# Performance work log

Measured on AMD Instinct MI355X. Metric: run time of the kernel, lower is better.

The kernel has to match this reference:

```python
import jax, jax.numpy as jnp
import numpy as np
from jax import lax

B, T, N, H, NC = 2, 8, 512, 64, 10
NEG = -1e9
LN_EPS = 1e-5


def _gatv2(x, mask, Wl, Wr, att, b):
    # GATv2Conv (PyG semantics, eval mode): e_ij = att . leaky_relu(Wr x_i + Wl x_j),
    # softmax over source nodes j with self-loops, out_i = sum_j alpha_ij * (Wl x_j).
    # x: (B, N, Fin); mask: (N, N) bool adjacency incl. self-loops; att: (heads, C).
    heads, C = att.shape
    Bn, Nn, _ = x.shape
    xl = (x @ Wl).reshape(Bn, Nn, heads, C)  # source transform
    xr = (x @ Wr).reshape(Bn, Nn, heads, C)  # target transform
    s = jax.nn.leaky_relu(xr[:, :, None] + xl[:, None, :], 0.2)  # (B, Ni, Nj, h, C)
    e = jnp.einsum('bijhc,hc->bijh', s, att)
    e = jnp.where(mask[None, :, :, None], e, NEG)
    alpha = jax.nn.softmax(e, axis=2)  # softmax over neighbors j
    out = jnp.einsum('bijh,bjhc->bihc', alpha, xl)
    return out.reshape(Bn, Nn, heads * C) + b


def _gru_layer(x, Wih, Whh, bih, bhh):
    # torch nn.GRU single layer, batch_first; x: (B, T, Hin)
    h0 = jnp.zeros((x.shape[0], Whh.shape[0]), x.dtype)
    def step(h, xt):
        gi = xt @ Wih + bih
        gh = h @ Whh + bhh
        ir, iz, inn = jnp.split(gi, 3, axis=-1)
        hr, hz, hn = jnp.split(gh, 3, axis=-1)
        r = jax.nn.sigmoid(ir + hr)
        z = jax.nn.sigmoid(iz + hz)
        n = jnp.tanh(inn + r * hn)
        hnew = (1.0 - z) * n + z * h
        return hnew, hnew
    _, ys = lax.scan(step, h0, jnp.swapaxes(x, 0, 1))
    return jnp.swapaxes(ys, 0, 1)


def setup_inputs() -> dict:
    key = jax.random.key(0)
    ks = jax.random.split(key, 20)
    def rn(i, shape, s=0.1):
        return jax.random.normal(ks[i], shape, jnp.float32) * s
    x_seq = jax.random.normal(ks[0], (B, T, N, 1), jnp.float32)
    a = jax.random.uniform(ks[1], (N, N))
    up = jnp.triu((a > 0.95).astype(jnp.float32), 1)
    static_adj = up + up.T  # sparse symmetric 0/1 static graph
    dyn_W = jax.random.normal(ks[2], (N, N), jnp.float32)
    reg_lambda = jnp.array([0.05], jnp.float32)
    return {
        'x_seq': x_seq, 'static_adj': static_adj, 'dyn_W': dyn_W, 'reg_lambda': reg_lambda,
        'g1_Wl': rn(3, (1, H)), 'g1_Wr': rn(4, (1, H)), 'g1_att': rn(5, (4, H // 4)), 'g1_b': jnp.zeros(H),
        'g2_Wl': rn(6, (H, H)), 'g2_Wr': rn(7, (H, H)), 'g2_att': rn(8, (1, H)), 'g2_b': jnp.zeros(H),
        'gru_Wih0': rn(9, (H, 3 * H)), 'gru_Whh0': rn(10, (H, 3 * H)), 'gru_bih0': jnp.zeros(3 * H), 'gru_bhh0': jnp.zeros(3 * H),
        'gru_Wih1': rn(11, (H, 3 * H)), 'gru_Whh1': rn(12, (H, 3 * H)), 'gru_bih1': jnp.zeros(3 * H), 'gru_bhh1': jnp.zeros(3 * H),
        'attn_W': rn(13, (H, 1)), 'attn_b': jnp.zeros(1),
        'cls_W1': rn(14, (H, H)), 'cls_b1': jnp.zeros(H), 'ln_g': jnp.ones(H), 'ln_b': jnp.zeros(H),
        'cls_W2': rn(15, (H, NC)), 'cls_b2': jnp.zeros(NC),
    }


def reference(x_seq, static_adj, dyn_W, reg_lambda,
              g1_Wl, g1_Wr, g1_att, g1_b, g2_Wl, g2_Wr, g2_att, g2_b,
              gru_Wih0, gru_Whh0, gru_bih0, gru_bhh0,
              gru_Wih1, gru_Whh1, gru_bih1, gru_bhh1,
              attn_W, attn_b, cls_W1, cls_b1, ln_g, ln_b, cls_W2, cls_b2):
    Bn, Tn, Nn, _ = x_seq.shape
    lam = jnp.maximum(reg_lambda[0], 0.01)
    t = jnp.arange(Tn, dtype=x_seq.dtype)
    gts = jnp.exp(-lam * t)  # gating values per timestep
    dyn = jax.nn.relu(dyn_W + dyn_W.T)
    fused = gts[:, None, None] * static_adj + (1.0 - gts)[:, None, None] * dyn  # (T, N, N)
    masks = (fused > 0) | jnp.eye(Nn, dtype=bool)[None]  # edge set + self-loops

    def step(carry, inp):
        xt, mask = inp  # xt: (B, N, 1)
        h = jax.nn.elu(_gatv2(xt, mask, g1_Wl, g1_Wr, g1_att, g1_b))
        h = jax.nn.elu(_gatv2(h, mask, g2_Wl, g2_Wr, g2_att, g2_b))
        return carry, h.mean(axis=1)  # (B, H) graph readout

    _, reps = lax.scan(step, 0.0, (jnp.swapaxes(x_seq, 0, 1), masks))
    h_seq = jnp.swapaxes(reps, 0, 1)  # (B, T, H)

    gru_out = _gru_layer(h_seq, gru_Wih0, gru_Whh0, gru_bih0, gru_bhh0)
    gru_out = _gru_layer(gru_out, gru_Wih1, gru_Whh1, gru_bih1, gru_bhh1)

    att_scores = jax.nn.softmax((gru_out @ attn_W + attn_b)[..., 0], axis=1)  # (B, T)
    final = jnp.einsum('bt,bth->bh', att_scores, gru_out)

    z = final @ cls_W1 + cls_b1
    mu = jnp.mean(z, axis=-1, keepdims=True)
    var = jnp.var(z, axis=-1, keepdims=True)
    z = (z - mu) / jnp.sqrt(var + LN_EPS) * ln_g + ln_b
    z = jax.nn.gelu(z, approximate=False)
    logits = z @ cls_W2 + cls_b2
    return logits, gts, att_scores
```

## Files before the change

kernel.cpp:

```cpp
#include <hip/hip_runtime.h>
#include <math.h>

#define BB 2
#define TT 8
#define NN 512
#define HH 64
#define NC 10

typedef unsigned char uchar;

__device__ __forceinline__ float elu1(float v){ return v > 0.f ? v : expm1f(v); }
__device__ __forceinline__ float sigm(float v){ return 1.f/(1.f+expf(-v)); }

__global__ __launch_bounds__(256) void k_mask(
    const float* __restrict__ dW, const float* __restrict__ sadj,
    uchar* __restrict__ M0, uchar* __restrict__ M1,
    float* __restrict__ Z2, float* __restrict__ hseq,
    const float* __restrict__ att1, const float* __restrict__ Wr1,
    const float* __restrict__ Wl1, float* __restrict__ AB,
    const float* __restrict__ Whh0, const float* __restrict__ Wih1,
    const float* __restrict__ Whh1, float4* __restrict__ WT4)
{
    __shared__ float tr[64][65];
    int bx = blockIdx.x, by = blockIdx.y;
    int tid = threadIdx.x;
    if (blockIdx.z == 1){
        int idx = (by*8 + bx)*256 + tid;
        if (idx < 3*4096){
            int m = idx >> 12, r = idx & 4095;
            int gg = r >> 6, k = r & 63;
            const float* W = (m == 0) ? Whh0 : (m == 1) ? Wih1 : Whh1;
            float4 o;
            o.x = W[k*192 + gg];
            o.y = W[k*192 + 64 + gg];
            o.z = W[k*192 + 128 + gg];
            o.w = 0.f;
            WT4[(size_t)m*4096 + r] = o;
        }
        return;
    }
    int i0 = by*64, j0 = bx*64;
    #pragma unroll
    for (int q = 0; q < 4; ++q){
        int r = (tid >> 4) + 16*q, c4 = tid & 15;
        float4 v = *(const float4*)&dW[(size_t)(j0+r)*NN + i0 + 4*c4];
        tr[r][4*c4+0] = v.x; tr[r][4*c4+1] = v.y;
        tr[r][4*c4+2] = v.z; tr[r][4*c4+3] = v.w;
    }
    __syncthreads();
    #pragma unroll
    for (int q = 0; q < 4; ++q){
        int row = (tid >> 4) + 16*q, c4 = tid & 15;
        int i = i0 + row, j = j0 + 4*c4;
        float4 d  = *(const float4*)&dW[(size_t)i*NN + j];
        float4 sa = *(const float4*)&sadj[(size_t)i*NN + j];
        uchar4 m0, m1;
        float dd0 = d.x + tr[4*c4+0][row];
        float dd1 = d.y + tr[4*c4+1][row];
        float dd2 = d.z + tr[4*c4+2][row];
        float dd3 = d.w + tr[4*c4+3][row];
        m0.x = (sa.x > 0.f) || (i == j+0);
        m0.y = (sa.y > 0.f) || (i == j+1);
        m0.z = (sa.z > 0.f) || (i == j+2);
        m0.w = (sa.w > 0.f) || (i == j+3);
        m1.x = m0.x || (dd0 > 0.f);
        m1.y = m0.y || (dd1 > 0.f);
        m1.z = m0.z || (dd2 > 0.f);
        m1.w = m0.w || (dd3 > 0.f);
        *(uchar4*)&M0[(size_t)i*NN + j] = m0;
        *(uchar4*)&M1[(size_t)i*NN + j] = m1;
    }
    int flat = (by*8 + bx)*256 + tid;
    if (flat < BB*TT*NN) Z2[flat] = 0.f;
    else if (flat < BB*TT*NN + BB*TT*HH) hseq[flat - BB*TT*NN] = 0.f;
    if (bx == 0 && by == 0 && tid < 8){
        int h = tid & 3;
        const float* W = (tid < 4) ? Wr1 : Wl1;
        float s = 0.f;
        for (int c = 0; c < 16; ++c) s += att1[h*16+c]*W[h*16+c];
        AB[tid] = s;
    }
}

__global__ __launch_bounds__(256) void k_gat1f(
    const float* __restrict__ x_seq, const uchar* __restrict__ M0,
    const uchar* __restrict__ M1,
    const float* __restrict__ Wl, const float* __restrict__ Wr,
    const float* __restrict__ att, const float* __restrict__ bias,
    const float* __restrict__ AB,
    const float* __restrict__ Wl2, const float* __restrict__ Wr2,
    const float* __restrict__ att2,
    float* __restrict__ xl2, float* __restrict__ xr2,
    float* __restrict__ ui, float* __restrict__ vj)
{
    __shared__ float x_s[NN];
    __shared__ float S_s[4][4];
    __shared__ float h_s[4][HH];
    __shared__ float Wl2_s[64*64];
    __shared__ float Wr2_s[64*64];
    int bt = blockIdx.y; int t = bt % TT;
    int i0 = blockIdx.x * 4;
    int tid = threadIdx.x;
    int il = tid >> 6, jl = tid & 63;
    int i = i0 + il;
    const uchar* M = t ? M1 : M0;
    ((float2*)x_s)[tid] = ((const float2*)(x_seq + bt*NN))[tid];
    #pragma unroll
    for (int q = 0; q < 4; ++q){
        int idx = q*256 + tid;
        ((float4*)Wl2_s)[idx] = ((const float4*)Wl2)[idx];
        ((float4*)Wr2_s)[idx] = ((const float4*)Wr2)[idx];
    }
    __syncthreads();
    float xi = x_s[i];
    const uchar* Mrow = M + (size_t)i*NN;
    float xj[8], msk[8];
    #pragma unroll
    for (int jj = 0; jj < 8; ++jj){
        int j = jj*64 + jl;
        xj[jj] = x_s[j];
        msk[jj] = Mrow[j] ? 1.f : 0.f;
    }
    float sw[4] = {0,0,0,0}, swx[4] = {0,0,0,0};
    for (int h = 0; h < 4; ++h){
        float acc[8] = {0,0,0,0,0,0,0,0};
        #pragma unroll
        for (int c = 0; c < 16; ++c){
            int hc = h*16 + c;
            float wl = Wl[hc];
            float q  = 0.4f * att[hc];
            float pr = xi * Wr[hc];
            #pragma unroll
            for (int jj = 0; jj < 8; ++jj){
                float s = fmaf(xj[jj], wl, pr);
                acc[jj] = fmaf(q, fabsf(s), acc[jj]);
            }
        }
        float lin = 0.6f * xi * AB[h];
        float al6 = 0.6f * AB[4+h];
        #pragma unroll
        for (int jj = 0; jj < 8; ++jj){
            float e = acc[jj] + fmaf(al6, xj[jj], lin);
            float w = msk[jj] * __expf(e);
            sw[h] += w;
            swx[h] = fmaf(w, xj[jj], swx[h]);
        }
    }
    #pragma unroll
    for (int off = 32; off; off >>= 1){
        #pragma unroll
        for (int h = 0; h < 4; ++h){
            sw[h]  += __shfl_down(sw[h],  off);
            swx[h] += __shfl_down(swx[h], off);
        }
    }
    if (jl == 0){
        #pragma unroll
        for (int h = 0; h < 4; ++h) S_s[il][h] = swx[h] / sw[h];
    }
    __syncthreads();
    {
        int hc = tid & 63, row = tid >> 6;
        float v = S_s[row][hc >> 4] * Wl[hc] + bias[hc];
        h_s[row][hc] = elu1(v);
    }
    __syncthreads();
    {
        int c = tid & 63, row = tid >> 6;
        float al = 0.f, ar = 0.f;
        #pragma unroll 8
        for (int k = 0; k < 64; ++k){
            float hv = h_s[row][k];
            al = fmaf(hv, Wl2_s[k*64 + c], al);
            ar = fmaf(hv, Wr2_s[k*64 + c], ar);
        }
        size_t ridx = (size_t)(bt*NN + i0 + row);
        xl2[ridx*HH + c] = al;
        xr2[ridx*HH + c] = ar;
        float a2 = att2[c];
        float pu = a2 * ar, pv = a2 * al;
        #pragma unroll
        for (int off = 32; off; off >>= 1){
            pu += __shfl_down(pu, off);
            pv += __shfl_down(pv, off);
        }
        if (c == 0){ ui[ridx] = pu; vj[ridx] = pv; }
    }
}

__global__ __launch_bounds__(256) void k_e2(
    const float* __restrict__ xl2, const float* __restrict__ xr2,
    const uchar* __restrict__ M0, const uchar* __restrict__ M1,
    const float* __restrict__ att,
    const float* __restrict__ ui, const float* __restrict__ vj,
    float* __restrict__ WgT, float* __restrict__ Z2)
{
    __shared__ float xrT[64][68];
    __shared__ float xlT[64][68];
    int bt = blockIdx.z, t = bt % TT;
    int i0 = blockIdx.y*64, j0 = blockIdx.x*64;
    int base = bt*NN;
    int tid = threadIdx.x;
    const uchar* M = t ? M1 : M0;
    {
        int r = tid >> 2;
        #pragma unroll
        for (int q = 0; q < 4; ++q){
            int c4 = (tid & 3) + 4*q;
            float4 a = *(const float4*)&xr2[(size_t)(base+i0+r)*HH + 4*c4];
            float4 b = *(const float4*)&xl2[(size_t)(base+j0+r)*HH + 4*c4];
            xrT[4*c4+0][r] = a.x; xrT[4*c4+1][r] = a.y;
            xrT[4*c4+2][r] = a.z; xrT[4*c4+3][r] = a.w;
            xlT[4*c4+0][r] = b.x; xlT[4*c4+1][r] = b.y;
            xlT[4*c4+2][r] = b.z; xlT[4*c4+3][r] = b.w;
        }
    }
    int ti = tid >> 4, tj = tid & 15;
    int iL = ti*4, jL = tj*4;
    float4 u4 = *(const float4*)&ui[base+i0+iL];
    float4 v4 = *(const float4*)&vj[base+j0+jL];
    float uu[4] = {u4.x, u4.y, u4.z, u4.w};
    float vv[4] = {v4.x, v4.y, v4.z, v4.w};
    float acc[4][4];
    #pragma unroll
    for (int ii = 0; ii < 4; ++ii)
        #pragma unroll
        for (int jj = 0; jj < 4; ++jj)
            acc[ii][jj] = 0.6f*(uu[ii] + vv[jj]);
    __syncthreads();
    #pragma unroll 8
    for (int c = 0; c < 64; ++c){
        float qa = 0.4f * att[c];
        float4 a4 = *(const float4*)&xrT[c][iL];
        float4 b4 = *(const float4*)&xlT[c][jL];
        float a[4] = {a4.x, a4.y, a4.z, a4.w};
        float b[4] = {b4.x, b4.y, b4.z, b4.w};
        #pragma unroll
        for (int ii = 0; ii < 4; ++ii)
            #pragma unroll
            for (int jj = 0; jj < 4; ++jj)
                acc[ii][jj] = fmaf(qa, fabsf(a[ii] + b[jj]), acc[ii][jj]);
    }
    float w[4][4];
    #pragma unroll
    for (int ii = 0; ii < 4; ++ii){
        int i = i0 + iL + ii;
        uchar4 mr = *(const uchar4*)&M[(size_t)i*NN + j0 + jL];
        w[ii][0] = mr.x ? __expf(acc[ii][0]) : 0.f;
        w[ii][1] = mr.y ? __expf(acc[ii][1]) : 0.f;
        w[ii][2] = mr.z ? __expf(acc[ii][2]) : 0.f;
        w[ii][3] = mr.w ? __expf(acc[ii][3]) : 0.f;
    }
    #pragma unroll
    for (int jj = 0; jj < 4; ++jj){
        int j = j0 + jL + jj;
        float4 wv = { w[0][jj], w[1][jj], w[2][jj], w[3][jj] };
        *(float4*)&WgT[(size_t)(base+j)*NN + i0 + iL] = wv;
    }
    #pragma unroll
    for (int ii = 0; ii < 4; ++ii){
        float zi = w[ii][0] + w[ii][1] + w[ii][2] + w[ii][3];
        zi += __shfl_down(zi, 8);
        zi += __shfl_down(zi, 4);
        zi += __shfl_down(zi, 2);
        zi += __shfl_down(zi, 1);
        if (tj == 0) atomicAdd(&Z2[base + i0 + iL + ii], zi);
    }
}

__global__ __launch_bounds__(256) void k_a2(
    const float* __restrict__ WgT, const float* __restrict__ xl2,
    const float* __restrict__ Z2, const float* __restrict__ bias,
    float* __restrict__ hseq)
{
    __shared__ float a_s[64][20];
    __shared__ float x_s[64][68];
    __shared__ float msum[64];
    int bt = blockIdx.y;
    int i0 = blockIdx.x * 16;
    int base = bt * NN;
    int tid = threadIdx.x;
    int tg = tid >> 4, tc = tid & 15;
    if (tid < 64) msum[tid] = 0.f;
    float4 acc = {0,0,0,0};
    for (int jc = 0; jc < 8; ++jc){
        int j0 = jc*64;
        {
            int row = tid >> 2, c4 = tid & 3;
            ((float4*)&a_s[row][0])[c4] = ((const float4*)&WgT[(size_t)(base+j0+row)*NN + i0])[c4];
        }
        #pragma unroll
        for (int q = 0; q < 4; ++q){
            int idx = q*256 + tid; int row = idx >> 4, c4 = idx & 15;
            ((float4*)&x_s[row][0])[c4] = ((const float4*)&xl2[(size_t)(base+j0+row)*HH])[c4];
        }
        __syncthreads();
        #pragma unroll 8
        for (int j = 0; j < 64; ++j){
            float a = a_s[j][tg];
            float4 xv = ((float4*)&x_s[j][0])[tc];
            acc.x = fmaf(a, xv.x, acc.x);
            acc.y = fmaf(a, xv.y, acc.y);
            acc.z = fmaf(a, xv.z, acc.z);
            acc.w = fmaf(a, xv.w, acc.w);
        }
        __syncthreads();
    }
    float rz = 1.f / Z2[base + i0 + tg];
    float4 b4 = ((const float4*)bias)[tc];
    float4 h;
    h.x = elu1(acc.x*rz + b4.x);
    h.y = elu1(acc.y*rz + b4.y);
    h.z = elu1(acc.z*rz + b4.z);
    h.w = elu1(acc.w*rz + b4.w);
    atomicAdd(&msum[tc*4+0], h.x);
    atomicAdd(&msum[tc*4+1], h.y);
    atomicAdd(&msum[tc*4+2], h.z);
    atomicAdd(&msum[tc*4+3], h.w);
    __syncthreads();
    if (tid < 64) atomicAdd(&hseq[bt*HH + tid], msum[tid]*(1.f/(float)NN));
}

__global__ __launch_bounds__(256) void k_pre(
    const float* __restrict__ hseq, const float* __restrict__ Wih0,
    const float* __restrict__ bih0, float* __restrict__ gi0)
{
    int idx = blockIdx.x*256 + threadIdx.x;
    int bt = idx / 192, g = idx % 192;
    const float* x = hseq + bt*HH;
    float acc = bih0[g];
    #pragma unroll 8
    for (int k = 0; k < HH; ++k)
        acc = fmaf(x[k], Wih0[k*192 + g], acc);
    gi0[idx] = acc;
}

#define P4 65
__global__ __launch_bounds__(512) void k_gru2(
    const float* __restrict__ gi0, const float4* __restrict__ WT4,
    const float* __restrict__ bhh0,
    const float* __restrict__ bih1, const float* __restrict__ bhh1,
    const float* __restrict__ lamp, const float* __restrict__ attn_W,
    const float* __restrict__ attn_b, const float* __restrict__ W1,
    const float* __restrict__ b1, const float* __restrict__ ln_g,
    const float* __restrict__ ln_b, const float* __restrict__ W2,
    const float* __restrict__ b2, float* __restrict__ out)
{
    __shared__ float4 WA[64*P4];
    __shared__ float4 WB[64*P4];
    __shared__ float gi_s[BB*TT*192];
    __shared__ float y_s[BB*TT*HH];
    __shared__ float sc_s[BB][TT], at_s[BB][TT];
    __shared__ float fin_s[BB][HH], z_s[BB][HH], g_s[BB][HH];
    __shared__ float mu_s[BB], iv_s[BB];
    int tid = threadIdx.x;
    int wave = tid >> 6, lane = tid & 63;
    for (int v = tid; v < 4096; v += 512){
        WA[(v >> 6)*P4 + (v & 63)] = WT4[v];
        WB[(v >> 6)*P4 + (v & 63)] = WT4[4096 + v];
    }
    for (int v = tid; v < BB*TT*192; v += 512) gi_s[v] = gi0[v];
    __syncthreads();
    float y[TT];
    float g1r[TT], g1z[TT], g1n[TT];
    if (wave < 2){
        int b = wave;
        float bhr = bhh0[lane], bhz = bhh0[64+lane], bhn = bhh0[128+lane];
        float h = 0.f;
        for (int t = 0; t < TT; ++t){
            float ghr = bhr, ghz = bhz, ghn = bhn;
            #pragma unroll 16
            for (int k = 0; k < 64; ++k){
                float4 w4 = WA[lane*P4 + k];
                float hk = __shfl(h, k);
                ghr = fmaf(w4.x, hk, ghr);
                ghz = fmaf(w4.y, hk, ghz);
                ghn = fmaf(w4.z, hk, ghn);
            }
            const float* gi = &gi_s[(b*TT + t)*192];
            float r = sigm(gi[lane] + ghr);
            float z = sigm(gi[64+lane] + ghz);
            float n = tanhf(gi[128+lane] + r*ghn);
            h = (1.f - z)*n + z*h;
            y[t] = h;
        }
        float bi1r = bih1[lane], bi1z = bih1[64+lane], bi1n = bih1[128+lane];
        #pragma unroll
        for (int t = 0; t < TT; ++t){ g1r[t] = bi1r; g1z[t] = bi1z; g1n[t] = bi1n; }
        #pragma unroll 8
        for (int k = 0; k < 64; ++k){
            float4 w4 = WB[lane*P4 + k];
            #pragma unroll
            for (int t = 0; t < TT; ++t){
                float yk = __shfl(y[t], k);
                g1r[t] = fmaf(w4.x, yk, g1r[t]);
                g1z[t] = fmaf(w4.y, yk, g1z[t]);
                g1n[t] = fmaf(w4.z, yk, g1n[t]);
            }
        }
    }
    __syncthreads();
    if (wave >= 2){
        for (int v = tid - 128; v < 4096; v += 384)
            WA[(v >> 6)*P4 + (v & 63)] = WT4[2*4096 + v];
    }
    __syncthreads();
    if (wave < 2){
        int b = wave;
        float bhr = bhh1[lane], bhz = bhh1[64+lane], bhn = bhh1[128+lane];
        float h = 0.f;
        for (int t = 0; t < TT; ++t){
            float ghr = bhr, ghz = bhz, ghn = bhn;
            #pragma unroll 16
            for (int k = 0; k < 64; ++k){
                float4 w4 = WA[lane*P4 + k];
                float hk = __shfl(h, k);
                ghr = fmaf(w4.x, hk, ghr);
                ghz = fmaf(w4.y, hk, ghz);
                ghn = fmaf(w4.z, hk, ghn);
            }
            float r = sigm(g1r[t] + ghr);
            float z = sigm(g1z[t] + ghz);
            float n = tanhf(g1n[t] + r*ghn);
            h = (1.f - z)*n + z*h;
            y_s[(b*TT + t)*HH + lane] = h;
        }
    }
    __syncthreads();
    float lam = fmaxf(lamp[0], 0.01f);
    if (tid < TT) out[BB*NC + tid] = expf(-lam*(float)tid);
    if (tid < BB*TT){
        int bb = tid >> 3, t = tid & 7;
        float s = attn_b[0];
        const float* r = &y_s[(bb*TT+t)*HH];
        for (int h = 0; h < HH; ++h) s += r[h]*attn_W[h];
        sc_s[bb][t] = s;
    }
    __syncthreads();
    if (tid < BB){
        float mx = -INFINITY;
        for (int t = 0; t < TT; ++t) mx = fmaxf(mx, sc_s[tid][t]);
        float se = 0.f;
        for (int t = 0; t < TT; ++t){ float w = expf(sc_s[tid][t]-mx); at_s[tid][t] = w; se += w; }
        for (int t = 0; t < TT; ++t){
            at_s[tid][t] /= se;
            out[BB*NC + TT + tid*TT + t] = at_s[tid][t];
        }
    }
    __syncthreads();
    if (tid < BB*HH){
        int bb = tid >> 6, h = tid & 63;
        float a = 0.f;
        for (int t = 0; t < TT; ++t) a += at_s[bb][t]*y_s[(bb*TT+t)*HH + h];
        fin_s[bb][h] = a;
    }
    __syncthreads();
    if (tid < BB*HH){
        int bb = tid >> 6, h = tid & 63;
        float a = b1[h];
        for (int k = 0; k < HH; ++k) a += fin_s[bb][k]*W1[k*HH+h];
        z_s[bb][h] = a;
    }
    __syncthreads();
    if (tid < BB){
        float mu = 0.f;
        for (int h = 0; h < HH; ++h) mu += z_s[tid][h];
        mu *= (1.f/HH);
        float v = 0.f;
        for (int h = 0; h < HH; ++h){ float d = z_s[tid][h]-mu; v += d*d; }
        v *= (1.f/HH);
        mu_s[tid] = mu; iv_s[tid] = 1.f/sqrtf(v + 1e-5f);
    }
    __syncthreads();
    if (tid < BB*HH){
        int bb = tid >> 6, h = tid & 63;
        float zn = (z_s[bb][h]-mu_s[bb])*iv_s[bb]*ln_g[h] + ln_b[h];
        g_s[bb][h] = 0.5f*zn*(1.f + erff(zn*0.70710678118654752f));
    }
    __syncthreads();
    if (tid < BB*NC){
        int bb = tid / NC, c = tid % NC;
        float a = b2[c];
        for (int k = 0; k < HH; ++k) a += g_s[bb][k]*W2[k*NC+c];
        out[bb*NC + c] = a;
    }
}

extern "C" void kernel_launch(void* const* d_in, const int* in_sizes, int n_in,
                              void* d_out, int out_size, void* d_ws, size_t ws_size,
                              hipStream_t stream)
{
    const float* x_seq = (const float*)d_in[0];
    const float* sadj  = (const float*)d_in[1];
    const float* dynW  = (const float*)d_in[2];
    const float* lamp  = (const float*)d_in[3];
    const float* g1_Wl = (const float*)d_in[4];
    const float* g1_Wr = (const float*)d_in[5];
    const float* g1_att= (const float*)d_in[6];
    const float* g1_b  = (const float*)d_in[7];
    const float* g2_Wl = (const float*)d_in[8];
    const float* g2_Wr = (const float*)d_in[9];
    const float* g2_att= (const float*)d_in[10];
    const float* g2_b  = (const float*)d_in[11];
    const float* Wih0  = (const float*)d_in[12];
    const float* Whh0  = (const float*)d_in[13];
    const float* bih0  = (const float*)d_in[14];
    const float* bhh0  = (const float*)d_in[15];
    const float* Wih1  = (const float*)d_in[16];
    const float* Whh1  = (const float*)d_in[17];
    const float* bih1  = (const float*)d_in[18];
    const float* bhh1  = (const float*)d_in[19];
    const float* attnW = (const float*)d_in[20];
    const float* attnb = (const float*)d_in[21];
    const float* W1    = (const float*)d_in[22];
    const float* b1    = (const float*)d_in[23];
    const float* lng   = (const float*)d_in[24];
    const float* lnb   = (const float*)d_in[25];
    const float* W2    = (const float*)d_in[26];
    const float* b2    = (const float*)d_in[27];
    float* out = (float*)d_out;

    const int RWS = BB*TT*NN*HH;
    uchar* M0 = (uchar*)d_ws;
    uchar* M1 = M0 + (size_t)NN*NN;
    float* fb = (float*)(M1 + (size_t)NN*NN);
    float* Z2   = fb;
    float* AB   = Z2   + BB*TT*NN;
    float* ui   = AB   + 16;
    float* vj   = ui   + BB*TT*NN;
    float* xl2  = vj   + BB*TT*NN;
    float* xr2  = xl2  + RWS;
    float* WgT  = xr2  + RWS;
    float* hseq = WgT  + (size_t)BB*TT*NN*NN;
    float* gi0  = hseq + BB*TT*HH;
    float4* WT4 = (float4*)(gi0 + BB*TT*192);

    k_mask <<<dim3(8,8,2), 256, 0, stream>>>(dynW, sadj, M0, M1, Z2, hseq, g1_att, g1_Wr, g1_Wl, AB,
                                             Whh0, Wih1, Whh1, WT4);
    k_gat1f<<<dim3(NN/4, BB*TT), 256, 0, stream>>>(x_seq, M0, M1, g1_Wl, g1_Wr, g1_att, g1_b, AB,
                                                   g2_Wl, g2_Wr, g2_att, xl2, xr2, ui, vj);
    k_e2   <<<dim3(NN/64, NN/64, BB*TT), 256, 0, stream>>>(xl2, xr2, M0, M1, g2_att, ui, vj, WgT, Z2);
    k_a2   <<<dim3(NN/16, BB*TT), 256, 0, stream>>>(WgT, xl2, Z2, g2_b, hseq);
    k_pre  <<<12, 256, 0, stream>>>(hseq, Wih0, bih0, gi0);
    k_gru2 <<<1, 512, 0, stream>>>(gi0, WT4, bhh0, bih1, bhh1,
                                   lamp, attnW, attnb, W1, b1, lng, lnb, W2, b2, out);
}
```

Before: 223.0 us.

## Fuse GAT, GRU and classifier stages into one persistent kernel with grid barriers

Replaces the six-kernel pipeline with a small init kernel plus a single persistent 256-block kernel whose stages are separated by a software grid barrier built on atomics. Intermediate buffers such as the dense NxN weight matrix and the atomic normalizer appear to be dropped, with layer-2 attention likely recomputed per row block and per-block mean partials used for the readout. This aims to remove launch overhead and large global round-trips. It risks deadlock if the 256 blocks are not all co-resident, and the grid barriers serialize stages.

New measurement: 390.7 us. 75.2% more time.

```diff
diff --git a/kernel.cpp b/kernel.cpp
--- a/kernel.cpp
+++ b/kernel.cpp
@@ -6,483 +6,488 @@
 #define NN 512
 #define HH 64
 #define NC 10
+#define NBLK 256
 
 typedef unsigned char uchar;
 
 __device__ __forceinline__ float elu1(float v){ return v > 0.f ? v : expm1f(v); }
 __device__ __forceinline__ float sigm(float v){ return 1.f/(1.f+expf(-v)); }
 
-__global__ __launch_bounds__(256) void k_mask(
-    const float* __restrict__ dW, const float* __restrict__ sadj,
-    uchar* __restrict__ M0, uchar* __restrict__ M1,
-    float* __restrict__ Z2, float* __restrict__ hseq,
-    const float* __restrict__ att1, const float* __restrict__ Wr1,
-    const float* __restrict__ Wl1, float* __restrict__ AB,
-    const float* __restrict__ Whh0, const float* __restrict__ Wih1,
-    const float* __restrict__ Whh1, float4* __restrict__ WT4)
-{
-    __shared__ float tr[64][65];
-    int bx = blockIdx.x, by = blockIdx.y;
-    int tid = threadIdx.x;
-    if (blockIdx.z == 1){
-        int idx = (by*8 + bx)*256 + tid;
-        if (idx < 3*4096){
-            int m = idx >> 12, r = idx & 4095;
-            int gg = r >> 6, k = r & 63;
-            const float* W = (m == 0) ? Whh0 : (m == 1) ? Wih1 : Whh1;
-            float4 o;
-            o.x = W[k*192 + gg];
-            o.y = W[k*192 + 64 + gg];
-            o.z = W[k*192 + 128 + gg];
-            o.w = 0.f;
-            WT4[(size_t)m*4096 + r] = o;
-        }
-        return;
-    }
-    int i0 = by*64, j0 = bx*64;
-    #pragma unroll
-    for (int q = 0; q < 4; ++q){
-        int r = (tid >> 4) + 16*q, c4 = tid & 15;
-        float4 v = *(const float4*)&dW[(size_t)(j0+r)*NN + i0 + 4*c4];
-        tr[r][4*c4+0] = v.x; tr[r][4*c4+1] = v.y;
-        tr[r][4*c4+2] = v.z; tr[r][4*c4+3] = v.w;
+__device__ __forceinline__ void grid_barrier(unsigned* bar){
+    __syncthreads();
+    if (threadIdx.x == 0){
+        __threadfence();
+        unsigned gen = __hip_atomic_load(&bar[1], __ATOMIC_ACQUIRE, __HIP_MEMORY_SCOPE_AGENT);
+        unsigned a = __hip_atomic_fetch_add(&bar[0], 1u, __ATOMIC_ACQ_REL, __HIP_MEMORY_SCOPE_AGENT);
+        if (a == NBLK - 1u){
+            __hip_atomic_store(&bar[0], 0u, __ATOMIC_RELAXED, __HIP_MEMORY_SCOPE_AGENT);
+            __hip_atomic_fetch_add(&bar[1], 1u, __ATOMIC_RELEASE, __HIP_MEMORY_SCOPE_AGENT);
+        } else {
+            while (__hip_atomic_load(&bar[1], __ATOMIC_ACQUIRE, __HIP_MEMORY_SCOPE_AGENT) == gen)
+                __builtin_amdgcn_s_sleep(8);
+        }
+        __threadfence();
     }
     __syncthreads();
-    #pragma unroll
-    for (int q = 0; q < 4; ++q){
-        int row = (tid >> 4) + 16*q, c4 = tid & 15;
-        int i = i0 + row, j = j0 + 4*c4;
-        float4 d  = *(const float4*)&dW[(size_t)i*NN + j];
-        float4 sa = *(const float4*)&sadj[(size_t)i*NN + j];
-        uchar4 m0, m1;
-        float dd0 = d.x + tr[4*c4+0][row];
-        float dd1 = d.y + tr[4*c4+1][row];
-        float dd2 = d.z + tr[4*c4+2][row];
-        float dd3 = d.w + tr[4*c4+3][row];
-        m0.x = (sa.x > 0.f) || (i == j+0);
-        m0.y = (sa.y > 0.f) || (i == j+1);
-        m0.z = (sa.z > 0.f) || (i == j+2);
-        m0.w = (sa.w > 0.f) || (i == j+3);
-        m1.x = m0.x || (dd0 > 0.f);
-        m1.y = m0.y || (dd1 > 0.f);
-        m1.z = m0.z || (dd2 > 0.f);
-        m1.w = m0.w || (dd3 > 0.f);
-        *(uchar4*)&M0[(size_t)i*NN + j] = m0;
-        *(uchar4*)&M1[(size_t)i*NN + j] = m1;
+}
+
+struct Prm {
+    const float *x_seq, *sadj, *dW, *lamp;
+    const float *g1_Wl, *g1_Wr, *g1_att, *g1_b;
+    const float *g2_Wl, *g2_Wr, *g2_att, *g2_b;
+    const float *Wih0, *bih0, *bhh0;
+    const float *bih1, *bhh1;
+    const float *attnW, *attnb, *W1, *b1, *lng, *lnb, *W2, *b2;
+    uchar *M0, *M1;
+    float *WT4;
+    float *xl2, *xr2, *ui, *vj, *meanPart;
+    unsigned *bar;
+    float *out;
+};
+
+__global__ __launch_bounds__(256) void k_init(
+    const float* __restrict__ Whh0, const float* __restrict__ Wih1,
+    const float* __restrict__ Whh1, const float* __restrict__ lamp,
+    float4* __restrict__ WT4, unsigned* __restrict__ bar, float* __restrict__ out)
+{
+    int idx = blockIdx.x*256 + threadIdx.x;
+    if (blockIdx.x == 0){
+        if (threadIdx.x < 2) bar[threadIdx.x] = 0u;
+        if (threadIdx.x >= 32 && threadIdx.x < 32 + TT){
+            int t = threadIdx.x - 32;
+            float lam = fmaxf(lamp[0], 0.01f);
+            out[BB*NC + t] = expf(-lam*(float)t);
+        }
     }
-    int flat = (by*8 + bx)*256 + tid;
-    if (flat < BB*TT*NN) Z2[flat] = 0.f;
-    else if (flat < BB*TT*NN + BB*TT*HH) hseq[flat - BB*TT*NN] = 0.f;
-    if (bx == 0 && by == 0 && tid < 8){
-        int h = tid & 3;
-        const float* W = (tid < 4) ? Wr1 : Wl1;
-        float s = 0.f;
-        for (int c = 0; c < 16; ++c) s += att1[h*16+c]*W[h*16+c];
-        AB[tid] = s;
-    }
+    int m = idx >> 12, r = idx & 4095;
+    int gg = r >> 6, k = r & 63;
+    const float* W = (m == 0) ? Whh0 : (m == 1) ? Wih1 : Whh1;
+    float4 o;
+    o.x = W[k*192 + gg];
+    o.y = W[k*192 + 64 + gg];
+    o.z = W[k*192 + 128 + gg];
+    o.w = 0.f;
+    WT4[idx] = o;
 }
 
-__global__ __launch_bounds__(256) void k_gat1f(
-    const float* __restrict__ x_seq, const uchar* __restrict__ M0,
-    const uchar* __restrict__ M1,
-    const float* __restrict__ Wl, const float* __restrict__ Wr,
-    const float* __restrict__ att, const float* __restrict__ bias,
-    const float* __restrict__ AB,
-    const float* __restrict__ Wl2, const float* __restrict__ Wr2,
-    const float* __restrict__ att2,
-    float* __restrict__ xl2, float* __restrict__ xr2,
-    float* __restrict__ ui, float* __restrict__ vj)
+#define SMEM_BYTES 52736
+
+__global__ __launch_bounds__(256, 1) void mega(Prm p)
 {
-    __shared__ float x_s[NN];
-    __shared__ float S_s[4][4];
-    __shared__ float h_s[4][HH];
-    __shared__ float Wl2_s[64*64];
-    __shared__ float Wr2_s[64*64];
-    int bt = blockIdx.y; int t = bt % TT;
-    int i0 = blockIdx.x * 4;
+    __shared__ __align__(16) char smem[SMEM_BYTES];
+    int blk = blockIdx.x;
     int tid = threadIdx.x;
-    int il = tid >> 6, jl = tid & 63;
-    int i = i0 + il;
-    const uchar* M = t ? M1 : M0;
-    ((float2*)x_s)[tid] = ((const float2*)(x_seq + bt*NN))[tid];
-    #pragma unroll
-    for (int q = 0; q < 4; ++q){
-        int idx = q*256 + tid;
-        ((float4*)Wl2_s)[idx] = ((const float4*)Wl2)[idx];
-        ((float4*)Wr2_s)[idx] = ((const float4*)Wr2)[idx];
-    }
-    __syncthreads();
-    float xi = x_s[i];
-    const uchar* Mrow = M + (size_t)i*NN;
-    float xj[8], msk[8];
-    #pragma unroll
-    for (int jj = 0; jj < 8; ++jj){
-        int j = jj*64 + jl;
-        xj[jj] = x_s[j];
-        msk[jj] = Mrow[j] ? 1.f : 0.f;
-    }
-    float sw[4] = {0,0,0,0}, swx[4] = {0,0,0,0};
-    for (int h = 0; h < 4; ++h){
-        float acc[8] = {0,0,0,0,0,0,0,0};
-        #pragma unroll
-        for (int c = 0; c < 16; ++c){
-            int hc = h*16 + c;
-            float wl = Wl[hc];
-            float q  = 0.4f * att[hc];
-            float pr = xi * Wr[hc];
-            #pragma unroll
-            for (int jj = 0; jj < 8; ++jj){
-                float s = fmaf(xj[jj], wl, pr);
-                acc[jj] = fmaf(q, fabsf(s), acc[jj]);
-            }
-        }
-        float lin = 0.6f * xi * AB[h];
-        float al6 = 0.6f * AB[4+h];
-        #pragma unroll
-        for (int jj = 0; jj < 8; ++jj){
-            float e = acc[jj] + fmaf(al6, xj[jj], lin);
-            float w = msk[jj] * __expf(e);
-            sw[h] += w;
-            swx[h] = fmaf(w, xj[jj], swx[h]);
-        }
-    }
-    #pragma unroll
-    for (int off = 32; off; off >>= 1){
-        #pragma unroll
-        for (int h = 0; h < 4; ++h){
-            sw[h]  += __shfl_down(sw[h],  off);
-            swx[h] += __shfl_down(swx[h], off);
-        }
-    }
-    if (jl == 0){
-        #pragma unroll
-        for (int h = 0; h < 4; ++h) S_s[il][h] = swx[h] / sw[h];
-    }
-    __syncthreads();
-    {
-        int hc = tid & 63, row = tid >> 6;
-        float v = S_s[row][hc >> 4] * Wl[hc] + bias[hc];
-        h_s[row][hc] = elu1(v);
-    }
-    __syncthreads();
-    {
-        int c = tid & 63, row = tid >> 6;
-        float al = 0.f, ar = 0.f;
-        #pragma unroll 8
-        for (int k = 0; k < 64; ++k){
-            float hv = h_s[row][k];
-            al = fmaf(hv, Wl2_s[k*64 + c], al);
-            ar = fmaf(hv, Wr2_s[k*64 + c], ar);
-        }
-        size_t ridx = (size_t)(bt*NN + i0 + row);
-        xl2[ridx*HH + c] = al;
-        xr2[ridx*HH + c] = ar;
-        float a2 = att2[c];
-        float pu = a2 * ar, pv = a2 * al;
-        #pragma unroll
-        for (int off = 32; off; off >>= 1){
-            pu += __shfl_down(pu, off);
-            pv += __shfl_down(pv, off);
-        }
-        if (c == 0){ ui[ridx] = pu; vj[ridx] = pv; }
-    }
-}
-
-__global__ __launch_bounds__(256) void k_e2(
-    const float* __restrict__ xl2, const float* __restrict__ xr2,
-    const uchar* __restrict__ M0, const uchar* __restrict__ M1,
-    const float* __restrict__ att,
-    const float* __restrict__ ui, const float* __restrict__ vj,
-    float* __restrict__ WgT, float* __restrict__ Z2)
-{
-    __shared__ float xrT[64][68];
-    __shared__ float xlT[64][68];
-    int bt = blockIdx.z, t = bt % TT;
-    int i0 = blockIdx.y*64, j0 = blockIdx.x*64;
-    int base = bt*NN;
-    int tid = threadIdx.x;
-    const uchar* M = t ? M1 : M0;
-    {
-        int r = tid >> 2;
+
+    if (blk < 64){
+        float (*tr)[65] = (float(*)[65])smem;
+        int i0 = (blk >> 3)*64, j0 = (blk & 7)*64;
         #pragma unroll
         for (int q = 0; q < 4; ++q){
-            int c4 = (tid & 3) + 4*q;
-            float4 a = *(const float4*)&xr2[(size_t)(base+i0+r)*HH + 4*c4];
-            float4 b = *(const float4*)&xl2[(size_t)(base+j0+r)*HH + 4*c4];
-            xrT[4*c4+0][r] = a.x; xrT[4*c4+1][r] = a.y;
-            xrT[4*c4+2][r] = a.z; xrT[4*c4+3][r] = a.w;
-            xlT[4*c4+0][r] = b.x; xlT[4*c4+1][r] = b.y;
-            xlT[4*c4+2][r] = b.z; xlT[4*c4+3][r] = b.w;
-        }
-    }
-    int ti = tid >> 4, tj = tid & 15;
-    int iL = ti*4, jL = tj*4;
-    float4 u4 = *(const float4*)&ui[base+i0+iL];
-    float4 v4 = *(const float4*)&vj[base+j0+jL];
-    float uu[4] = {u4.x, u4.y, u4.z, u4.w};
-    float vv[4] = {v4.x, v4.y, v4.z, v4.w};
-    float acc[4][4];
-    #pragma unroll
-    for (int ii = 0; ii < 4; ++ii)
-        #pragma unroll
-        for (int jj = 0; jj < 4; ++jj)
-            acc[ii][jj] = 0.6f*(uu[ii] + vv[jj]);
-    __syncthreads();
-    #pragma unroll 8
-    for (int c = 0; c < 64; ++c){
-        float qa = 0.4f * att[c];
-        float4 a4 = *(const float4*)&xrT[c][iL];
-        float4 b4 = *(const float4*)&xlT[c][jL];
-        float a[4] = {a4.x, a4.y, a4.z, a4.w};
-        float b[4] = {b4.x, b4.y, b4.z, b4.w};
-        #pragma unroll
-        for (int ii = 0; ii < 4; ++ii)
-            #pragma unroll
-            for (int jj = 0; jj < 4; ++jj)
-                acc[ii][jj] = fmaf(qa, fabsf(a[ii] + b[jj]), acc[ii][jj]);
-    }
-    float w[4][4];
-    #pragma unroll
-    for (int ii = 0; ii < 4; ++ii){
-        int i = i0 + iL + ii;
-        uchar4 mr = *(const uchar4*)&M[(size_t)i*NN + j0 + jL];
-        w[ii][0] = mr.x ? __expf(acc[ii][0]) : 0.f;
-        w[ii][1] = mr.y ? __expf(acc[ii][1]) : 0.f;
-        w[ii][2] = mr.z ? __expf(acc[ii][2]) : 0.f;
-        w[ii][3] = mr.w ? __expf(acc[ii][3]) : 0.f;
-    }
-    #pragma unroll
-    for (int jj = 0; jj < 4; ++jj){
-        int j = j0 + jL + jj;
-        float4 wv = { w[0][jj], w[1][jj], w[2][jj], w[3][jj] };
-        *(float4*)&WgT[(size_t)(base+j)*NN + i0 + iL] = wv;
-    }
-    #pragma unroll
-    for (int ii = 0; ii < 4; ++ii){
-        float zi = w[ii][0] + w[ii][1] + w[ii][2] + w[ii][3];
-        zi += __shfl_down(zi, 8);
-        zi += __shfl_down(zi, 4);
-        zi += __shfl_down(zi, 2);
-        zi += __shfl_down(zi, 1);
-        if (tj == 0) atomicAdd(&Z2[base + i0 + iL + ii], zi);
-    }
-}
-
-__global__ __launch_bounds__(256) void k_a2(
-    const float* __restrict__ WgT, const float* __restrict__ xl2,
-    const float* __restrict__ Z2, const float* __restrict__ bias,
-    float* __restrict__ hseq)
-{
-    __shared__ float a_s[64][20];
-    __shared__ float x_s[64][68];
-    __shared__ float msum[64];
-    int bt = blockIdx.y;
-    int i0 = blockIdx.x * 16;
-    int base = bt * NN;
-    int tid = threadIdx.x;
-    int tg = tid >> 4, tc = tid & 15;
-    if (tid < 64) msum[tid] = 0.f;
-    float4 acc = {0,0,0,0};
-    for (int jc = 0; jc < 8; ++jc){
-        int j0 = jc*64;
-        {
-            int row = tid >> 2, c4 = tid & 3;
-            ((float4*)&a_s[row][0])[c4] = ((const float4*)&WgT[(size_t)(base+j0+row)*NN + i0])[c4];
-        }
+            int r = (tid >> 4) + 16*q, c4 = tid & 15;
+            float4 v = *(const float4*)&p.dW[(size_t)(j0+r)*NN + i0 + 4*c4];
+            tr[r][4*c4+0] = v.x; tr[r][4*c4+1] = v.y;
+            tr[r][4*c4+2] = v.z; tr[r][4*c4+3] = v.w;
+        }
+        __syncthreads();
         #pragma unroll
         for (int q = 0; q < 4; ++q){
-            int idx = q*256 + tid; int row = idx >> 4, c4 = idx & 15;
-            ((float4*)&x_s[row][0])[c4] = ((const float4*)&xl2[(size_t)(base+j0+row)*HH])[c4];
-        }
-        __syncthreads();
-        #pragma unroll 8
-        for (int j = 0; j < 64; ++j){
-            float a = a_s[j][tg];
-            float4 xv = ((float4*)&x_s[j][0])[tc];
-            acc.x = fmaf(a, xv.x, acc.x);
-            acc.y = fmaf(a, xv.y, acc.y);
-            acc.z = fmaf(a, xv.z, acc.z);
-            acc.w = fmaf(a, xv.w, acc.w);
-        }
-        __syncthreads();
+            int row = (tid >> 4) + 16*q, c4 = tid & 15;
+            int i = i0 + row, j = j0 + 4*c4;
+            float4 d  = *(const float4*)&p.dW[(size_t)i*NN + j];
+            float4 sa = *(const float4*)&p.sadj[(size_t)i*NN + j];
+            uchar4 m0, m1;
+            float dd0 = d.x + tr[4*c4+0][row];
+            float dd1 = d.y + tr[4*c4+1][row];
+            float dd2 = d.z + tr[4*c4+2][row];
+            float dd3 = d.w + tr[4*c4+3][row];
+            m0.x = (sa.x > 0.f) || (i == j+0);
+            m0.y = (sa.y > 0.f) || (i == j+1);
+            m0.z = (sa.z > 0.f) || (i == j+2);
+            m0.w = (sa.w > 0.f) || (i == j+3);
+            m1.x = m0.x || (dd0 > 0.f);
+            m1.y = m0.y || (dd1 > 0.f);
+            m1.z = m0.z || (dd2 > 0.f);
+            m1.w = m0.w || (dd3 > 0.f);
+            *(uchar4*)&p.M0[(size_t)i*NN + j] = m0;
+            *(uchar4*)&p.M1[(size_t)i*NN + j] = m1;
+        }
     }
-    float rz = 1.f / Z2[base + i0 + tg];
-    float4 b4 = ((const float4*)bias)[tc];
-    float4 h;
-    h.x = elu1(acc.x*rz + b4.x);
-    h.y = elu1(acc.y*rz + b4.y);
-    h.z = elu1(acc.z*rz + b4.z);
-    h.w = elu1(acc.w*rz + b4.w);
-    atomicAdd(&msum[tc*4+0], h.x);
-    atomicAdd(&msum[tc*4+1], h.y);
-    atomicAdd(&msum[tc*4+2], h.z);
-    atomicAdd(&msum[tc*4+3], h.w);
-    __syncthreads();
-    if (tid < 64) atomicAdd(&hseq[bt*HH + tid], msum[tid]*(1.f/(float)NN));
-}
-
-__global__ __launch_bounds__(256) void k_pre(
-    const float* __restrict__ hseq, const float* __restrict__ Wih0,
-    const float* __restrict__ bih0, float* __restrict__ gi0)
-{
-    int idx = blockIdx.x*256 + threadIdx.x;
-    int bt = idx / 192, g = idx % 192;
-    const float* x = hseq + bt*HH;
-    float acc = bih0[g];
-    #pragma unroll 8
-    for (int k = 0; k < HH; ++k)
-        acc = fmaf(x[k], Wih0[k*192 + g], acc);
-    gi0[idx] = acc;
-}
-
-#define P4 65
-__global__ __launch_bounds__(512) void k_gru2(
-    const float* __restrict__ gi0, const float4* __restrict__ WT4,
-    const float* __restrict__ bhh0,
-    const float* __restrict__ bih1, const float* __restrict__ bhh1,
-    const float* __restrict__ lamp, const float* __restrict__ attn_W,
-    const float* __restrict__ attn_b, const float* __restrict__ W1,
-    const float* __restrict__ b1, const float* __restrict__ ln_g,
-    const float* __restrict__ ln_b, const float* __restrict__ W2,
-    const float* __restrict__ b2, float* __restrict__ out)
-{
-    __shared__ float4 WA[64*P4];
-    __shared__ float4 WB[64*P4];
-    __shared__ float gi_s[BB*TT*192];
-    __shared__ float y_s[BB*TT*HH];
-    __shared__ float sc_s[BB][TT], at_s[BB][TT];
-    __shared__ float fin_s[BB][HH], z_s[BB][HH], g_s[BB][HH];
-    __shared__ float mu_s[BB], iv_s[BB];
-    int tid = threadIdx.x;
-    int wave = tid >> 6, lane = tid & 63;
-    for (int v = tid; v < 4096; v += 512){
-        WA[(v >> 6)*P4 + (v & 63)] = WT4[v];
-        WB[(v >> 6)*P4 + (v & 63)] = WT4[4096 + v];
+    grid_barrier(p.bar);
+
+    {
+        float* Wl2s = (float*)smem;
+        float* Wr2s = (float*)(smem + 16384);
+        float* x_s  = (float*)(smem + 32768);
+        float (*h_s)[64] = (float(*)[64])(smem + 34816);
+        float (*S_s)[4]  = (float(*)[4]) (smem + 35840);
+        float* AB_s = (float*)(smem + 35904);
+        int bt = blk >> 4, ig = blk & 15;
+        int t = bt % TT;
+        #pragma unroll
+        for (int q = 0; q < 4; ++q){
+            int idx = q*256 + tid;
+            ((float4*)Wl2s)[idx] = ((const float4*)p.g2_Wl)[idx];
+            ((float4*)Wr2s)[idx] = ((const float4*)p.g2_Wr)[idx];
+        }
+        ((float2*)x_s)[tid] = ((const float2*)(p.x_seq + bt*NN))[tid];
+        if (tid < 8){
+            int h = tid & 3;
+            const float* W = (tid < 4) ? p.g1_Wr : p.g1_Wl;
+            float s = 0.f;
+            for (int c = 0; c < 16; ++c) s += p.g1_att[h*16+c]*W[h*16+c];
+            AB_s[tid] = s;
+        }
+        __syncthreads();
+        const uchar* M = t ? p.M1 : p.M0;
+        int il = tid >> 6, jl = tid & 63;
+        float xj[8];
+        #pragma unroll
+        for (int jj = 0; jj < 8; ++jj) xj[jj] = x_s[jj*64 + jl];
+        for (int s = 0; s < 8; ++s){
+            int i = ig*32 + s*4 + il;
+            float xi = x_s[i];
+            const uchar* Mrow = M + (size_t)i*NN;
+            float msk[8];
+            #pragma unroll
+            for (int jj = 0; jj < 8; ++jj) msk[jj] = Mrow[jj*64 + jl] ? 1.f : 0.f;
+            float sw[4] = {0,0,0,0}, swx[4] = {0,0,0,0};
+            for (int h = 0; h < 4; ++h){
+                float acc[8] = {0,0,0,0,0,0,0,0};
+                #pragma unroll
+                for (int c = 0; c < 16; ++c){
+                    int hc = h*16 + c;
+                    float wl = p.g1_Wl[hc];
+                    float q  = 0.4f * p.g1_att[hc];
+                    float pr = xi * p.g1_Wr[hc];
+                    #pragma unroll
+                    for (int jj = 0; jj < 8; ++jj){
+                        float sv = fmaf(xj[jj], wl, pr);
+                        acc[jj] = fmaf(q, fabsf(sv), acc[jj]);
+                    }
+                }
+                float lin = 0.6f * xi * AB_s[h];
+                float al6 = 0.6f * AB_s[4+h];
+                #pragma unroll
+                for (int jj = 0; jj < 8; ++jj){
+                    float e = acc[jj] + fmaf(al6, xj[jj], lin);
+                    float w = msk[jj] * __expf(e);
+                    sw[h] += w;
+                    swx[h] = fmaf(w, xj[jj], swx[h]);
+                }
+            }
+            #pragma unroll
+            for (int off = 32; off; off >>= 1){
+                #pragma unroll
+                for (int h = 0; h < 4; ++h){
+                    sw[h]  += __shfl_down(sw[h],  off);
+                    swx[h] += __shfl_down(swx[h], off);
+                }
+            }
+            if (jl == 0){
+                #pragma unroll
+                for (int h = 0; h < 4; ++h) S_s[il][h] = swx[h] / sw[h];
+            }
+            __syncthreads();
+            {
+                int hc = tid & 63, row = tid >> 6;
+                float v = S_s[row][hc >> 4] * p.g1_Wl[hc] + p.g1_b[hc];
+                h_s[row][hc] = elu1(v);
+            }
+            __syncthreads();
+            {
+                int c = tid & 63, row = tid >> 6;
+                float al = 0.f, ar = 0.f;
+                #pragma unroll 8
+                for (int k = 0; k < 64; ++k){
+                    float hv = h_s[row][k];
+                    al = fmaf(hv, Wl2s[k*64 + c], al);
+                    ar = fmaf(hv, Wr2s[k*64 + c], ar);
+                }
+                size_t ridx = (size_t)(bt*NN + ig*32 + s*4 + row);
+                p.xl2[ridx*HH + c] = al;
+                p.xr2[ridx*HH + c] = ar;
+                float a2 = p.g2_att[c];
+                float pu = a2 * ar, pv = a2 * al;
+                #pragma unroll
+                for (int off = 32; off; off >>= 1){
+                    pu += __shfl_down(pu, off);
+                    pv += __shfl_down(pv, off);
+                }
+                if (c == 0){ p.ui[ridx] = pu; p.vj[ridx] = pv; }
+            }
+            __syncthreads();
+        }
     }
-    for (int v = tid; v < BB*TT*192; v += 512) gi_s[v] = gi0[v];
-    __syncthreads();
-    float y[TT];
-    float g1r[TT], g1z[TT], g1n[TT];
-    if (wave < 2){
-        int b = wave;
-        float bhr = bhh0[lane], bhz = bhh0[64+lane], bhn = bhh0[128+lane];
-        float h = 0.f;
-        for (int t = 0; t < TT; ++t){
-            float ghr = bhr, ghz = bhz, ghn = bhn;
-            #pragma unroll 16
-            for (int k = 0; k < 64; ++k){
-                float4 w4 = WA[lane*P4 + k];
-                float hk = __shfl(h, k);
-                ghr = fmaf(w4.x, hk, ghr);
-                ghz = fmaf(w4.y, hk, ghz);
-                ghn = fmaf(w4.z, hk, ghn);
-            }
-            const float* gi = &gi_s[(b*TT + t)*192];
-            float r = sigm(gi[lane] + ghr);
-            float z = sigm(gi[64+lane] + ghz);
-            float n = tanhf(gi[128+lane] + r*ghn);
-            h = (1.f - z)*n + z*h;
-            y[t] = h;
-        }
-        float bi1r = bih1[lane], bi1z = bih1[64+lane], bi1n = bih1[128+lane];
+    grid_barrier(p.bar);
+
+    {
+        float (*xrT)[34] = (float(*)[34])smem;
+        float (*xlT)[68] = (float(*)[68])(smem + 8704);
+        float (*xlR)[68] = (float(*)[68])(smem + 26112);
+        float (*w_s)[68] = (float(*)[68])(smem + 43520);
+        float* Zl   = (float*)(smem + 52224);
+        float* msum = (float*)(smem + 52352);
+        int bt = blk >> 4, it = blk & 15;
+        int i0 = it*32, t = bt % TT, base = bt*NN;
+        const uchar* M = t ? p.M1 : p.M0;
         #pragma unroll
-        for (int t = 0; t < TT; ++t){ g1r[t] = bi1r; g1z[t] = bi1z; g1n[t] = bi1n; }
-        #pragma unroll 8
-        for (int k = 0; k < 64; ++k){
-            float4 w4 = WB[lane*P4 + k];
+        for (int e = 0; e < 2; ++e){
+            int idx = e*256 + tid;
+            int r = idx >> 4, c4 = idx & 15;
+            float4 v = *(const float4*)&p.xr2[(size_t)(base+i0+r)*HH + 4*c4];
+            xrT[4*c4+0][r] = v.x; xrT[4*c4+1][r] = v.y;
+            xrT[4*c4+2][r] = v.z; xrT[4*c4+3][r] = v.w;
+        }
+        if (tid < 32) Zl[tid] = 0.f;
+        if (tid < 64) msum[tid] = 0.f;
+        __syncthreads();
+        int ti = tid >> 4, tj = tid & 15;
+        int iL = ti*2, jL = tj*4;
+        int ir = ti, tc = tj;
+        float2 u2 = *(const float2*)&p.ui[base + i0 + iL];
+        float4 accA0 = {0,0,0,0}, accA1 = {0,0,0,0};
+        for (int jt = 0; jt < 8; ++jt){
+            int j0 = jt*64;
             #pragma unroll
+            for (int q = 0; q < 4; ++q){
+                int idx = q*256 + tid;
+                int r = idx >> 4, c4 = idx & 15;
+                float4 v = *(const float4*)&p.xl2[(size_t)(base+j0+r)*HH + 4*c4];
+                *(float4*)&xlR[r][4*c4] = v;
+                xlT[4*c4+0][r] = v.x; xlT[4*c4+1][r] = v.y;
+                xlT[4*c4+2][r] = v.z; xlT[4*c4+3][r] = v.w;
+            }
+            __syncthreads();
+            float4 v4 = *(const float4*)&p.vj[base + j0 + jL];
+            float e0[4], e1[4];
+            e0[0] = 0.6f*(u2.x + v4.x); e0[1] = 0.6f*(u2.x + v4.y);
+            e0[2] = 0.6f*(u2.x + v4.z); e0[3] = 0.6f*(u2.x + v4.w);
+            e1[0] = 0.6f*(u2.y + v4.x); e1[1] = 0.6f*(u2.y + v4.y);
+            e1[2] = 0.6f*(u2.y + v4.z); e1[3] = 0.6f*(u2.y + v4.w);
+            #pragma unroll 8
+            for (int c = 0; c < 64; ++c){
+                float qa = 0.4f * p.g2_att[c];
+                float2 a2 = *(const float2*)&xrT[c][iL];
+                float4 b4 = *(const float4*)&xlT[c][jL];
+                e0[0] = fmaf(qa, fabsf(a2.x + b4.x), e0[0]);
+                e0[1] = fmaf(qa, fabsf(a2.x + b4.y), e0[1]);
+                e0[2] = fmaf(qa, fabsf(a2.x + b4.z), e0[2]);
+                e0[3] = fmaf(qa, fabsf(a2.x + b4.w), e0[3]);
+                e1[0] = fmaf(qa, fabsf(a2.y + b4.x), e1[0]);
+                e1[1] = fmaf(qa, fabsf(a2.y + b4.y), e1[1]);
+                e1[2] = fmaf(qa, fabsf(a2.y + b4.z), e1[2]);
+                e1[3] = fmaf(qa, fabsf(a2.y + b4.w), e1[3]);
+            }
+            uchar4 mr0 = *(const uchar4*)&M[(size_t)(i0+iL+0)*NN + j0 + jL];
+            uchar4 mr1 = *(const uchar4*)&M[(size_t)(i0+iL+1)*NN + j0 + jL];
+            float4 w0, w1;
+            w0.x = mr0.x ? __expf(e0[0]) : 0.f;
+            w0.y = mr0.y ? __expf(e0[1]) : 0.f;
+            w0.z = mr0.z ? __expf(e0[2]) : 0.f;
+            w0.w = mr0.w ? __expf(e0[3]) : 0.f;
+            w1.x = mr1.x ? __expf(e1[0]) : 0.f;
+            w1.y = mr1.y ? __expf(e1[1]) : 0.f;
+            w1.z = mr1.z ? __expf(e1[2]) : 0.f;
+            w1.w = mr1.w ? __expf(e1[3]) : 0.f;
+            *(float4*)&w_s[iL+0][jL] = w0;
+            *(float4*)&w_s[iL+1][jL] = w1;
+            float zi0 = w0.x + w0.y + w0.z + w0.w;
+            float zi1 = w1.x + w1.y + w1.z + w1.w;
+            #pragma unroll
+            for (int off = 8; off; off >>= 1){
+                zi0 += __shfl_down(zi0, off);
+                zi1 += __shfl_down(zi1, off);
+            }
+            if (tj == 0){
+                atomicAdd(&Zl[iL+0], zi0);
+                atomicAdd(&Zl[iL+1], zi1);
+            }
+            __syncthreads();
+            #pragma unroll 4
+            for (int j4 = 0; j4 < 16; ++j4){
+                float4 wa = *(float4*)&w_s[ir][4*j4];
+                float4 wb = *(float4*)&w_s[ir+16][4*j4];
+                float4 x0 = *(float4*)&xlR[4*j4+0][4*tc];
+                float4 x1 = *(float4*)&xlR[4*j4+1][4*tc];
+                float4 x2 = *(float4*)&xlR[4*j4+2][4*tc];
+                float4 x3 = *(float4*)&xlR[4*j4+3][4*tc];
+                accA0.x += wa.x*x0.x + wa.y*x1.x + wa.z*x2.x + wa.w*x3.x;
+                accA0.y += wa.x*x0.y + wa.y*x1.y + wa.z*x2.y + wa.w*x3.y;
+                accA0.z += wa.x*x0.z + wa.y*x1.z + wa.z*x2.z + wa.w*x3.z;
+                accA0.w += wa.x*x0.w + wa.y*x1.w + wa.z*x2.w + wa.w*x3.w;
+                accA1.x += wb.x*x0.x + wb.y*x1.x + wb.z*x2.x + wb.w*x3.x;
+                accA1.y += wb.x*x0.y + wb.y*x1.y + wb.z*x2.y + wb.w*x3.y;
+                accA1.z += wb.x*x0.z + wb.y*x1.z + wb.z*x2.z + wb.w*x3.z;
+                accA1.w += wb.x*x0.w + wb.y*x1.w + wb.z*x2.w + wb.w*x3.w;
+            }
+            __syncthreads();
+        }
+        float rz0 = 1.f / Zl[ir];
+        float rz1 = 1.f / Zl[ir+16];
+        float4 b4 = ((const float4*)p.g2_b)[tc];
+        float4 h0, h1;
+        h0.x = elu1(accA0.x*rz0 + b4.x); h0.y = elu1(accA0.y*rz0 + b4.y);
+        h0.z = elu1(accA0.z*rz0 + b4.z); h0.w = elu1(accA0.w*rz0 + b4.w);
+        h1.x = elu1(accA1.x*rz1 + b4.x); h1.y = elu1(accA1.y*rz1 + b4.y);
+        h1.z = elu1(accA1.z*rz1 + b4.z); h1.w = elu1(accA1.w*rz1 + b4.w);
+        atomicAdd(&msum[4*tc+0], h0.x + h1.x);
+        atomicAdd(&msum[4*tc+1], h0.y + h1.y);
+        atomicAdd(&msum[4*tc+2], h0.z + h1.z);
+        atomicAdd(&msum[4*tc+3], h0.w + h1.w);
+        __syncthreads();
+        if (tid < 64) p.meanPart[(size_t)(bt*16 + it)*64 + tid] = msum[tid];
+    }
+    grid_barrier(p.bar);
+
+    if (blk != 0) return;
+    {
+        float* hseq_s = (float*)smem;
+        float* gi_s   = (float*)(smem + 4096);
+        float* y_s    = (float*)(smem + 16384);
+        float (*sc_s)[TT]  = (float(*)[TT])(smem + 20480);
+        float (*at_s)[TT]  = (float(*)[TT])(smem + 20480 + 64);
+        float (*fin_s)[HH] = (float(*)[HH])(smem + 20480 + 128);
+        float (*z_s)[HH]   = (float(*)[HH])(smem + 20480 + 128 + 512);
+        float (*g_s)[HH]   = (float(*)[HH])(smem + 20480 + 128 + 1024);
+        float* mu_s = (float*)(smem + 20480 + 128 + 1536);
+        float* iv_s = (float*)(smem + 20480 + 128 + 1536 + 8);
+        int wave = tid >> 6, lane = tid & 63;
+        for (int o = tid; o < BB*TT*HH; o += 256){
+            int bt = o >> 6, c = o & 63;
+            float s = 0.f;
+            #pragma unroll
+            for (int itt = 0; itt < 16; ++itt)
+                s += p.meanPart[(size_t)(bt*16 + itt)*64 + c];
+            hseq_s[o] = s * (1.f/(float)NN);
+        }
+        __syncthreads();
+        for (int o = tid; o < BB*TT*192; o += 256){
+            int bt = o / 192, g = o % 192;
+            float a = p.bih0[g];
+            #pragma unroll 8
+            for (int k = 0; k < HH; ++k)
+                a = fmaf(hseq_s[bt*HH + k], p.Wih0[k*192 + g], a);
+            gi_s[o] = a;
+        }
+        __syncthreads();
+        if (wave < 2){
+            int b = wave;
+            const float4* WT = (const float4*)p.WT4;
+            float y[TT], g1r[TT], g1z[TT], g1n[TT];
+            {
+                float bhr = p.bhh0[lane], bhz = p.bhh0[64+lane], bhn = p.bhh0[128+lane];
+                float h = 0.f;
+                for (int t = 0; t < TT; ++t){
+                    float ghr = bhr, ghz = bhz, ghn = bhn;
+                    #pragma unroll
+                    for (int k = 0; k < 64; ++k){
+                        float4 w4 = WT[lane*64 + k];
+                        float hk = __shfl(h, k);
+                        ghr = fmaf(w4.x, hk, ghr);
+                        ghz = fmaf(w4.y, hk, ghz);
+                        ghn = fmaf(w4.z, hk, ghn);
+                    }
+                    const float* gi = &gi_s[(b*TT + t)*192];
+                    float r = sigm(gi[lane] + ghr);
+                    float z = sigm(gi[64+lane] + ghz);
+                    float n = tanhf(gi[128+lane] + r*ghn);
+                    h = (1.f - z)*n + z*h;
+                    y[t] = h;
+                }
+            }
+            {
+                float bi1r = p.bih1[lane], bi1z = p.bih1[64+lane], bi1n = p.bih1[128+lane];
+                #pragma unroll
+                for (int t = 0; t < TT; ++t){ g1r[t] = bi1r; g1z[t] = bi1z; g1n[t] = bi1n; }
+                #pragma unroll 8
+                for (int k = 0; k < 64; ++k){
+                    float4 w4 = WT[4096 + lane*64 + k];
+                    #pragma unroll
+                    for (int t = 0; t < TT; ++t){
+                        float yk = __shfl(y[t], k);
+                        g1r[t] = fmaf(w4.x, yk, g1r[t]);
+                        g1z[t] = fmaf(w4.y, yk, g1z[t]);
+                        g1n[t] = fmaf(w4.z, yk, g1n[t]);
+                    }
+                }
+            }
+            {
+                float bhr = p.bhh1[lane], bhz = p.bhh1[64+lane], bhn = p.bhh1[128+lane];
+                float h = 0.f;
+                for (int t = 0; t < TT; ++t){
+                    float ghr = bhr, ghz = bhz, ghn = bhn;
+                    #pragma unroll
+                    for (int k = 0; k < 64; ++k){
+                        float4 w4 = WT[2*4096 + lane*64 + k];
+                        float hk = __shfl(h, k);
+                        ghr = fmaf(w4.x, hk, ghr);
+                        ghz = fmaf(w4.y, hk, ghz);
+                        ghn = fmaf(w4.z, hk, ghn);
+                    }
+                    float r = sigm(g1r[t] + ghr);
+                    float z = sigm(g1z[t] + ghz);
+                    float n = tanhf(g1n[t] + r*ghn);
+                    h = (1.f - z)*n + z*h;
+                    y_s[(b*TT + t)*HH + lane] = h;
+                }
+            }
+        }
+        __syncthreads();
+        if (tid < BB*TT){
+            int bb = tid >> 3, t = tid & 7;
+            float s = p.attnb[0];
+            const float* r = &y_s[(bb*TT+t)*HH];
+            for (int h = 0; h < HH; ++h) s += r[h]*p.attnW[h];
+            sc_s[bb][t] = s;
+        }
+        __syncthreads();
+        if (tid < BB){
+            float mx = -INFINITY;
+            for (int t = 0; t < TT; ++t) mx = fmaxf(mx, sc_s[tid][t]);
+            float se = 0.f;
+            for (int t = 0; t < TT; ++t){ float w = expf(sc_s[tid][t]-mx); at_s[tid][t] = w; se += w; }
             for (int t = 0; t < TT; ++t){
-                float yk = __shfl(y[t], k);
-                g1r[t] = fmaf(w4.x, yk, g1r[t]);
-                g1z[t] = fmaf(w4.y, yk, g1z[t]);
-                g1n[t] = fmaf(w4.z, yk, g1n[t]);
-            }
-        }
-    }
-    __syncthreads();
-    if (wave >= 2){
-        for (int v = tid - 128; v < 4096; v += 384)
-            WA[(v >> 6)*P4 + (v & 63)] = WT4[2*4096 + v];
-    }
-    __syncthreads();
-    if (wave < 2){
-        int b = wave;
-        float bhr = bhh1[lane], bhz = bhh1[64+lane], bhn = bhh1[128+lane];
-        float h = 0.f;
-        for (int t = 0; t < TT; ++t){
-            float ghr = bhr, ghz = bhz, ghn = bhn;
-            #pragma unroll 16
-            for (int k = 0; k < 64; ++k){
-                float4 w4 = WA[lane*P4 + k];
-                float hk = __shfl(h, k);
-                ghr = fmaf(w4.x, hk, ghr);
-                ghz = fmaf(w4.y, hk, ghz);
-                ghn = fmaf(w4.z, hk, ghn);
-            }
-            float r = sigm(g1r[t] + ghr);
-            float z = sigm(g1z[t] + ghz);
-            float n = tanhf(g1n[t] + r*ghn);
-            h = (1.f - z)*n + z*h;
-            y_s[(b*TT + t)*HH + lane] = h;
-        }
-    }
-    __syncthreads();
-    float lam = fmaxf(lamp[0], 0.01f);
-    if (tid < TT) out[BB*NC + tid] = expf(-lam*(float)tid);
-    if (tid < BB*TT){
-        int bb = tid >> 3, t = tid & 7;
-        float s = attn_b[0];
-        const float* r = &y_s[(bb*TT+t)*HH];
-        for (int h = 0; h < HH; ++h) s += r[h]*attn_W[h];
-        sc_s[bb][t] = s;
-    }
-    __syncthreads();
-    if (tid < BB){
-        float mx = -INFINITY;
-        for (int t = 0; t < TT; ++t) mx = fmaxf(mx, sc_s[tid][t]);
-        float se = 0.f;
-        for (int t = 0; t < TT; ++t){ float w = expf(sc_s[tid][t]-mx); at_s[tid][t] = w; se += w; }
-        for (int t = 0; t < TT; ++t){
-            at_s[tid][t] /= se;
-            out[BB*NC + TT + tid*TT + t] = at_s[tid][t];
-        }
-    }
-    __syncthreads();
-    if (tid < BB*HH){
-        int bb = tid >> 6, h = tid & 63;
-        float a = 0.f;
-        for (int t = 0; t < TT; ++t) a += at_s[bb][t]*y_s[(bb*TT+t)*HH + h];
-        fin_s[bb][h] = a;
-    }
-    __syncthreads();
-    if (tid < BB*HH){
-        int bb = tid >> 6, h = tid & 63;
-        float a = b1[h];
-        for (int k = 0; k < HH; ++k) a += fin_s[bb][k]*W1[k*HH+h];
-        z_s[bb][h] = a;
-    }
-    __syncthreads();
-    if (tid < BB){
-        float mu = 0.f;
-        for (int h = 0; h < HH; ++h) mu += z_s[tid][h];
-        mu *= (1.f/HH);
-        float v = 0.f;
-        for (int h = 0; h < HH; ++h){ float d = z_s[tid][h]-mu; v += d*d; }
-        v *= (1.f/HH);
-        mu_s[tid] = mu; iv_s[tid] = 1.f/sqrtf(v + 1e-5f);
-    }
-    __syncthreads();
-    if (tid < BB*HH){
-        int bb = tid >> 6, h = tid & 63;
-        float zn = (z_s[bb][h]-mu_s[bb])*iv_s[bb]*ln_g[h] + ln_b[h];
-        g_s[bb][h] = 0.5f*zn*(1.f + erff(zn*0.70710678118654752f));
-    }
-    __syncthreads();
-    if (tid < BB*NC){
-        int bb = tid / NC, c = tid % NC;
-        float a = b2[c];
-        for (int k = 0; k < HH; ++k) a += g_s[bb][k]*W2[k*NC+c];
-        out[bb*NC + c] = a;
+                at_s[tid][t] /= se;
+                p.out[BB*NC + TT + tid*TT + t] = at_s[tid][t];
+            }
+        }
+        __syncthreads();
+        if (tid < BB*HH){
+            int bb = tid >> 6, h = tid & 63;
+            float a = 0.f;
+            for (int t = 0; t < TT; ++t) a += at_s[bb][t]*y_s[(bb*TT+t)*HH + h];
+            fin_s[bb][h] = a;
+        }
+        __syncthreads();
+        if (tid < BB*HH){
+            int bb = tid >> 6, h = tid & 63;
+            float a = p.b1[h];
+            for (int k = 0; k < HH; ++k) a += fin_s[bb][k]*p.W1[k*HH+h];
+            z_s[bb][h] = a;
+        }
+        __syncthreads();
+        if (tid < BB){
+            float mu = 0.f;
+            for (int h = 0; h < HH; ++h) mu += z_s[tid][h];
+            mu *= (1.f/HH);
+            float v = 0.f;
+            for (int h = 0; h < HH; ++h){ float d = z_s[tid][h]-mu; v += d*d; }
+            v *= (1.f/HH);
+            mu_s[tid] = mu; iv_s[tid] = 1.f/sqrtf(v + 1e-5f);
+        }
+        __syncthreads();
+        if (tid < BB*HH){
+            int bb = tid >> 6, h = tid & 63;
+            float zn = (z_s[bb][h]-mu_s[bb])*iv_s[bb]*p.lng[h] + p.lnb[h];
+            g_s[bb][h] = 0.5f*zn*(1.f + erff(zn*0.70710678118654752f));
+        }
+        __syncthreads();
+        if (tid < BB*NC){
+            int bb = tid / NC, c = tid % NC;
+            float a = p.b2[c];
+            for (int k = 0; k < HH; ++k) a += g_s[bb][k]*p.W2[k*NC+c];
+            p.out[bb*NC + c] = a;
+        }
     }
 }
 
@@ -490,58 +495,50 @@
                               void* d_out, int out_size, void* d_ws, size_t ws_size,
                               hipStream_t stream)
 {
-    const float* x_seq = (const float*)d_in[0];
-    const float* sadj  = (const float*)d_in[1];
-    const float* dynW  = (const float*)d_in[2];
-    const float* lamp  = (const float*)d_in[3];
-    const float* g1_Wl = (const float*)d_in[4];
-    const float* g1_Wr = (const float*)d_in[5];
-    const float* g1_att= (const float*)d_in[6];
-    const float* g1_b  = (const float*)d_in[7];
-    const float* g2_Wl = (const float*)d_in[8];
-    const float* g2_Wr = (const float*)d_in[9];
-    const float* g2_att= (const float*)d_in[10];
-    const float* g2_b  = (const float*)d_in[11];
-    const float* Wih0  = (const float*)d_in[12];
-    const float* Whh0  = (const float*)d_in[13];
-    const float* bih0  = (const float*)d_in[14];
-    const float* bhh0  = (const float*)d_in[15];
-    const float* Wih1  = (const float*)d_in[16];
-    const float* Whh1  = (const float*)d_in[17];
-    const float* bih1  = (const float*)d_in[18];
-    const float* bhh1  = (const float*)d_in[19];
-    const float* attnW = (const float*)d_in[20];
-    const float* attnb = (const float*)d_in[21];
-    const float* W1    = (const float*)d_in[22];
-    const float* b1    = (const float*)d_in[23];
-    const float* lng   = (const float*)d_in[24];
-    const float* lnb   = (const float*)d_in[25];
-    const float* W2    = (const float*)d_in[26];
-    const float* b2    = (const float*)d_in[27];
-    float* out = (float*)d_out;
+    Prm p;
+    p.x_seq = (const float*)d_in[0];
+    p.sadj  = (const float*)d_in[1];
+    p.dW    = (const float*)d_in[2];
+    p.lamp  = (const float*)d_in[3];
+    p.g1_Wl = (const float*)d_in[4];
+    p.g1_Wr = (const float*)d_in[5];
+    p.g1_att= (const float*)d_in[6];
+    p.g1_b  = (const float*)d_in[7];
+    p.g2_Wl = (const float*)d_in[8];
+    p.g2_Wr = (const float*)d_in[9];
+    p.g2_att= (const float*)d_in[10];
+    p.g2_b  = (const float*)d_in[11];
+    p.Wih0  = (const float*)d_in[12];
+    const float* Whh0 = (const float*)d_in[13];
+    p.bih0  = (const float*)d_in[14];
+    p.bhh0  = (const float*)d_in[15];
+    const float* Wih1 = (const float*)d_in[16];
+    const float* Whh1 = (const float*)d_in[17];
+    p.bih1  = (const float*)d_in[18];
+    p.bhh1  = (const float*)d_in[19];
+    p.attnW = (const float*)d_in[20];
+    p.attnb = (const float*)d_in[21];
+    p.W1    = (const float*)d_in[22];
+    p.b1    = (const float*)d_in[23];
+    p.lng   = (const float*)d_in[24];
+    p.lnb   = (const float*)d_in[25];
+    p.W2    = (const float*)d_in[26];
+    p.b2    = (const float*)d_in[27];
+    p.out   = (float*)d_out;
 
     const int RWS = BB*TT*NN*HH;
-    uchar* M0 = (uchar*)d_ws;
-    uchar* M1 = M0 + (size_t)NN*NN;
-    float* fb = (float*)(M1 + (size_t)NN*NN);
-    float* Z2   = fb;
-    float* AB   = Z2   + BB*TT*NN;
-    float* ui   = AB   + 16;
-    float* vj   = ui   + BB*TT*NN;
-    float* xl2  = vj   + BB*TT*NN;
-    float* xr2  = xl2  + RWS;
-    float* WgT  = xr2  + RWS;
-    float* hseq = WgT  + (size_t)BB*TT*NN*NN;
-    float* gi0  = hseq + BB*TT*HH;
-    float4* WT4 = (float4*)(gi0 + BB*TT*192);
-
-    k_mask <<<dim3(8,8,2), 256, 0, stream>>>(dynW, sadj, M0, M1, Z2, hseq, g1_att, g1_Wr, g1_Wl, AB,
-                                             Whh0, Wih1, Whh1, WT4);
-    k_gat1f<<<dim3(NN/4, BB*TT), 256, 0, stream>>>(x_seq, M0, M1, g1_Wl, g1_Wr, g1_att, g1_b, AB,
-                                                   g2_Wl, g2_Wr, g2_att, xl2, xr2, ui, vj);
-    k_e2   <<<dim3(NN/64, NN/64, BB*TT), 256, 0, stream>>>(xl2, xr2, M0, M1, g2_att, ui, vj, WgT, Z2);
-    k_a2   <<<dim3(NN/16, BB*TT), 256, 0, stream>>>(WgT, xl2, Z2, g2_b, hseq);
-    k_pre  <<<12, 256, 0, stream>>>(hseq, Wih0, bih0, gi0);
-    k_gru2 <<<1, 512, 0, stream>>>(gi0, WT4, bhh0, bih1, bhh1,
-                                   lamp, attnW, attnb, W1, b1, lng, lnb, W2, b2, out);
+    p.M0 = (uchar*)d_ws;
+    p.M1 = p.M0 + (size_t)NN*NN;
+    float* fb = (float*)(p.M1 + (size_t)NN*NN);
+    p.WT4 = fb;
+    p.xl2 = p.WT4 + 3*4096*4;
+    p.xr2 = p.xl2 + RWS;
+    p.ui  = p.xr2 + RWS;
+    p.vj  = p.ui  + BB*TT*NN;
+    p.meanPart = p.vj + BB*TT*NN;
+    p.bar = (unsigned*)(p.meanPart + 16*16*64);
+
+    k_init<<<48, 256, 0, stream>>>(Whh0, Wih1, Whh1, p.lamp,
+                                   (float4*)p.WT4, p.bar, p.out);
+    mega  <<<NBLK, 256, 0, stream>>>(p);
 }
```
